# Kernel tuning notes

Hardware: AMD Instinct MI355X
Metric: run time of the kernel (lower is better)

The kernel has to match this reference:

```python
import jax, jax.numpy as jnp
import numpy as np

K1 = 3                      # spline kernel size per pseudo dim
SIZE = float(np.sqrt(2.0))  # pseudo_cartesian normalization size


def spline_weights(p, k):
    """Degree-1 open B-spline basis over 2D pseudo coords.
    p: [..., 2] in [0,1]. Returns basis [..., 4], weight_index [..., 4]."""
    v = jnp.clip(p, 0.0, 1.0) * (k - 1)
    lo = jnp.floor(v)
    frac = v - lo
    lo = lo.astype(jnp.int32)
    off = jnp.array([0, 1], dtype=jnp.int32)
    w0 = jnp.stack([1.0 - frac[..., 0], frac[..., 0]], axis=-1)   # [...,2]
    w1 = jnp.stack([1.0 - frac[..., 1], frac[..., 1]], axis=-1)   # [...,2]
    i0 = jnp.clip(lo[..., 0:1] + off, 0, k - 1)                    # [...,2]
    i1 = jnp.clip(lo[..., 1:2] + off, 0, k - 1)                    # [...,2]
    basis = (w0[..., :, None] * w1[..., None, :]).reshape(*p.shape[:-1], 4)
    widx = (i0[..., :, None] + k * i1[..., None, :]).reshape(*p.shape[:-1], 4)
    return basis, widx


def setup_inputs() -> dict:
    key = jax.random.key(0)
    kx, ke, kp, kq, kw, kb = jax.random.split(key, 6)
    N, C, P, E, K = 50000, 64, 16, 800000, K1 * K1
    x = jax.random.normal(kx, (N, C), dtype=jnp.float32)
    pos = jax.random.uniform(kp, (N, 2), dtype=jnp.float32)
    pose = jax.random.normal(kq, (N, P, 2), dtype=jnp.float32)
    pose = pose / (jnp.linalg.norm(pose, axis=-1, keepdims=True) + 1e-8)  # unit pose vectors
    W = jax.random.normal(kw, (P, K, C), dtype=jnp.float32) / np.sqrt(C * 4.0)
    bias = jax.random.normal(kb, (P,), dtype=jnp.float32) * 0.01
    edge_index = jax.random.randint(ke, (2, E), 0, N, dtype=jnp.int64)
    return {"x": x, "pos": pos, "pose": pose, "W": W, "bias": bias,
            "edge_index": edge_index}


def reference(x, pos, pose, W, bias, edge_index):
    N, C = x.shape
    P = pose.shape[1]
    row, col = edge_index[0], edge_index[1]
    # pseudo_cartesian: normalized relative position in [0,1]^2
    pseudo = (pos[col] - pos[row]) / (2.0 * SIZE) + 0.5              # [E,2]
    # posevec_to_rotmat on detached pose vectors
    pose_c = jax.lax.stop_gradient(pose)
    a, b = pose_c[..., 0], pose_c[..., 1]
    R = jnp.stack([jnp.stack([a, -b], -1), jnp.stack([b, a], -1)], -2)  # [N,P,2,2]
    Re = R[row]                                                      # [E,P,2,2]
    # rotate pseudo coords about (0.5, 0.5), batched over all poses
    p = jnp.einsum('epij,ej->epi', Re, pseudo - 0.5) + 0.5           # [E,P,2]
    basis, widx = spline_weights(p, K1)                              # [E,P,4]
    # SplineConv (out_channels=1, no root weight, no norm):
    # precompute per-node per-pose per-kernel-bin projections
    Z = jnp.einsum('nc,pkc->npk', x, W)                              # [N,P,K]
    pidx = jnp.arange(P)[None, :, None]
    vals = Z[col[:, None, None], pidx, widx]                         # [E,P,4]
    msg = jnp.sum(basis * vals, axis=-1)                             # [E,P]
    out = jax.ops.segment_sum(msg, row, num_segments=N)              # [N,P]
    return out + bias[None, :]
```

## Files before the change

kernel.cpp:

```cpp
#include <hip/hip_runtime.h>
#include <hip/hip_bf16.h>

#define C_DIM 64
#define P_DIM 16
#define K_DIM 9
#define PK (P_DIM * K_DIM)
#define INV2S 0.35355339059327373f

#define ZS_STRIDE 152
#define SH_FLOATS 4864

__global__ __launch_bounds__(256) void z_gemm_kernel(const float* __restrict__ x,
                                                     const float* __restrict__ W,
                                                     const float* __restrict__ bias,
                                                     float* __restrict__ out,
                                                     __hip_bfloat16* __restrict__ Zb,
                                                     int N) {
    __shared__ float sh_raw[SH_FLOATS];
    float (*xs)[C_DIM + 4] = (float(*)[C_DIM + 4])sh_raw;
    __hip_bfloat16* zs = (__hip_bfloat16*)sh_raw;

    const int block_row = blockIdx.x * 64;
    const int tid = threadIdx.x;

    {
        const float4 b4 = ((const float4*)bias)[tid & 3];
        const int o4 = block_row * 4 + tid;
        if (o4 < N * 4) ((float4*)out)[o4] = b4;
    }

    for (int i = tid; i < C_DIM * (C_DIM / 4); i += 256) {
        int r = i >> 4, c4 = i & 15;
        int gr = block_row + r;
        float4 v = make_float4(0.0f, 0.0f, 0.0f, 0.0f);
        if (gr < N) v = ((const float4*)x)[(size_t)gr * (C_DIM / 4) + c4];
        *(float4*)&xs[r][c4 * 4] = v;
    }
    __syncthreads();

    const int rg = tid & 15;
    const int p  = tid >> 4;
    const int j0 = p * K_DIM;

    float acc[4][K_DIM];
    #pragma unroll
    for (int i = 0; i < 4; ++i)
        #pragma unroll
        for (int k = 0; k < K_DIM; ++k) acc[i][k] = 0.0f;

    const float4* W4 = (const float4*)W;
    #pragma unroll 4
    for (int cs = 0; cs < 16; ++cs) {
        float4 xv[4];
        #pragma unroll
        for (int i = 0; i < 4; ++i) xv[i] = *(const float4*)&xs[rg + 16 * i][cs * 4];
        #pragma unroll
        for (int k = 0; k < K_DIM; ++k) {
            float4 wv = W4[(size_t)(j0 + k) * (C_DIM / 4) + cs];
            #pragma unroll
            for (int i = 0; i < 4; ++i) {
                acc[i][k] = fmaf(xv[i].x, wv.x, acc[i][k]);
                acc[i][k] = fmaf(xv[i].y, wv.y, acc[i][k]);
                acc[i][k] = fmaf(xv[i].z, wv.z, acc[i][k]);
                acc[i][k] = fmaf(xv[i].w, wv.w, acc[i][k]);
            }
        }
    }
    __syncthreads();

    #pragma unroll
    for (int i = 0; i < 4; ++i) {
        __hip_bfloat16* zrow = &zs[(rg + 16 * i) * ZS_STRIDE + j0];
        #pragma unroll
        for (int k = 0; k < K_DIM; ++k)
            zrow[k] = __float2bfloat16(acc[i][k]);
    }
    __syncthreads();

    const int nrow = min(64, N - block_row);
    float4* Zb4 = (float4*)Zb;
    for (int i = tid; i < nrow * 18; i += 256) {
        int row = i / 18, q = i - row * 18;
        float4 v = *(const float4*)&zs[row * ZS_STRIDE + q * 8];
        Zb4[(size_t)(block_row + row) * 18 + q] = v;
    }
}

#define EILP 8
__global__ __launch_bounds__(256) void edge_kernel(const int* __restrict__ ei,
                                                   const float* __restrict__ pos,
                                                   const float* __restrict__ pose,
                                                   const __hip_bfloat16* __restrict__ Zb,
                                                   float* __restrict__ out,
                                                   int E) {
    const int p  = threadIdx.x & 15;
    const int eg = threadIdx.x >> 4;
    const int e0 = blockIdx.x * (16 * EILP) + eg;

    int  r[EILP], c[EILP];
    bool valid[EILP];
    #pragma unroll
    for (int it = 0; it < EILP; ++it) {
        int e = e0 + it * 16;
        valid[it] = (e < E);
        int ec = valid[it] ? e : 0;
        r[it] = ei[ec];
        c[it] = ei[E + ec];
    }

    float d0[EILP], d1[EILP];
    #pragma unroll
    for (int it = 0; it < EILP; ++it) {
        const float2 pc = ((const float2*)pos)[c[it]];
        const float2 pr = ((const float2*)pos)[r[it]];
        d0[it] = (pc.x - pr.x) * INV2S;
        d1[it] = (pc.y - pr.y) * INV2S;
    }

    float2 ab[EILP];
    #pragma unroll
    for (int it = 0; it < EILP; ++it)
        ab[it] = ((const float2*)pose)[(size_t)r[it] * P_DIM + p];

    #pragma unroll
    for (int it = 0; it < EILP; ++it) {
        const float p0 = fmaf(ab[it].x, d0[it], fmaf(-ab[it].y, d1[it], 0.5f));
        const float p1 = fmaf(ab[it].y, d0[it], fmaf( ab[it].x, d1[it], 0.5f));

        const float v0 = fminf(fmaxf(p0, 0.0f), 1.0f) * 2.0f;
        const float v1 = fminf(fmaxf(p1, 0.0f), 1.0f) * 2.0f;
        const float lo0 = floorf(v0);
        const float lo1 = floorf(v1);
        const float f0 = v0 - lo0;
        const float f1 = v1 - lo1;
        const int i00 = min((int)lo0, 2);
        const int i01 = min((int)lo0 + 1, 2);
        const int i10 = min((int)lo1, 2);
        const int i11 = min((int)lo1 + 1, 2);

        const __hip_bfloat16* __restrict__ Zp = Zb + (size_t)c[it] * PK + p * K_DIM;
        const float w00 = (1.0f - f0) * (1.0f - f1);
        const float w01 = (1.0f - f0) * f1;
        const float w10 = f0 * (1.0f - f1);
        const float w11 = f0 * f1;

        float m = w00 * __bfloat162float(Zp[i00 + 3 * i10]);
        m = fmaf(w01, __bfloat162float(Zp[i00 + 3 * i11]), m);
        m = fmaf(w10, __bfloat162float(Zp[i01 + 3 * i10]), m);
        m = fmaf(w11, __bfloat162float(Zp[i01 + 3 * i11]), m);

        if (valid[it]) atomicAdd(&out[(size_t)r[it] * P_DIM + p], m);
    }
}

extern "C" void kernel_launch(void* const* d_in, const int* in_sizes, int n_in,
                              void* d_out, int out_size, void* d_ws, size_t ws_size,
                              hipStream_t stream) {
    const float* x    = (const float*)d_in[0];
    const float* pos  = (const float*)d_in[1];
    const float* pose = (const float*)d_in[2];
    const float* W    = (const float*)d_in[3];
    const float* bias = (const float*)d_in[4];
    const int*   ei   = (const int*)d_in[5];

    const int N = in_sizes[0] / C_DIM;
    const int E = in_sizes[5] / 2;

    float* out = (float*)d_out;
    __hip_bfloat16* Zb = (__hip_bfloat16*)d_ws;

    z_gemm_kernel<<<(N + 63) / 64, 256, 0, stream>>>(x, W, bias, out, Zb, N);
    edge_kernel<<<(E + 16 * EILP - 1) / (16 * EILP), 256, 0, stream>>>(ei, pos, pose, Zb, out, E);
}
```

Measured before the change: 156.0 us.

## Use split-bf16 MFMA for Z projection and bf16-packed pose for edge gather

The per-node projection GEMM is rewritten to use MFMA 16x16x32 bf16 instructions, with x and W each split into hi/lo bf16 parts so the product stays near fp32 accuracy. W is converted into shared memory per block, and Z is written straight from the accumulators. The GEMM kernel also packs pose vectors into bf16 pairs in workspace, halving the per-edge pose gather bytes in the edge kernel. This costs extra MFMA passes and redundant W conversion in every block, and pose precision drops to bf16.

Result: faster. 144.7 us (-7.2%).

```diff
diff --git a/kernel.cpp b/kernel.cpp
--- a/kernel.cpp
+++ b/kernel.cpp
@@ -1,5 +1,4 @@
 #include <hip/hip_runtime.h>
-#include <hip/hip_bf16.h>
 
 #define C_DIM 64
 #define P_DIM 16
@@ -7,21 +6,32 @@
 #define PK (P_DIM * K_DIM)
 #define INV2S 0.35355339059327373f
 
-#define ZS_STRIDE 152
-#define SH_FLOATS 4864
+typedef __attribute__((ext_vector_type(8))) short short8v;
+typedef __attribute__((ext_vector_type(4))) float f32x4;
+
+__device__ __forceinline__ ushort f2bf(float f) {
+    uint u = __builtin_bit_cast(uint, f);
+    return (ushort)((u + 0x7FFFu + ((u >> 16) & 1u)) >> 16);
+}
+__device__ __forceinline__ float bf2f(ushort h) {
+    return __builtin_bit_cast(float, ((uint)h) << 16);
+}
+
+#define ZSTRIDE 72
 
 __global__ __launch_bounds__(256) void z_gemm_kernel(const float* __restrict__ x,
                                                      const float* __restrict__ W,
                                                      const float* __restrict__ bias,
+                                                     const float* __restrict__ pose,
                                                      float* __restrict__ out,
-                                                     __hip_bfloat16* __restrict__ Zb,
+                                                     ushort* __restrict__ Zb,
+                                                     uint* __restrict__ pose_bf,
                                                      int N) {
-    __shared__ float sh_raw[SH_FLOATS];
-    float (*xs)[C_DIM + 4] = (float(*)[C_DIM + 4])sh_raw;
-    __hip_bfloat16* zs = (__hip_bfloat16*)sh_raw;
-
+    __shared__ ushort w_hi[PK * ZSTRIDE];
+    __shared__ ushort w_lo[PK * ZSTRIDE];
+
+    const int tid = threadIdx.x;
     const int block_row = blockIdx.x * 64;
-    const int tid = threadIdx.x;
 
     {
         const float4 b4 = ((const float4*)bias)[tid & 3];
@@ -29,68 +39,95 @@
         if (o4 < N * 4) ((float4*)out)[o4] = b4;
     }
 
-    for (int i = tid; i < C_DIM * (C_DIM / 4); i += 256) {
-        int r = i >> 4, c4 = i & 15;
-        int gr = block_row + r;
-        float4 v = make_float4(0.0f, 0.0f, 0.0f, 0.0f);
-        if (gr < N) v = ((const float4*)x)[(size_t)gr * (C_DIM / 4) + c4];
-        *(float4*)&xs[r][c4 * 4] = v;
+    if (pose_bf != nullptr) {
+        for (int i = tid; i < 64 * P_DIM; i += 256) {
+            const int r = block_row + (i >> 4);
+            if (r < N) {
+                const float2 ab = ((const float2*)pose)[(size_t)r * P_DIM + (i & 15)];
+                pose_bf[(size_t)r * P_DIM + (i & 15)] =
+                    (uint)f2bf(ab.x) | ((uint)f2bf(ab.y) << 16);
+            }
+        }
+    }
+
+    for (int i = tid; i < PK * (C_DIM / 2); i += 256) {
+        const int n  = i >> 5;
+        const int k2 = i & 31;
+        const float2 w2 = ((const float2*)W)[i];
+        const int o = n * ZSTRIDE + k2 * 2;
+        const ushort h0 = f2bf(w2.x);
+        const ushort h1 = f2bf(w2.y);
+        w_hi[o]     = h0;
+        w_hi[o + 1] = h1;
+        w_lo[o]     = f2bf(w2.x - bf2f(h0));
+        w_lo[o + 1] = f2bf(w2.y - bf2f(h1));
     }
     __syncthreads();
 
-    const int rg = tid & 15;
-    const int p  = tid >> 4;
-    const int j0 = p * K_DIM;
-
-    float acc[4][K_DIM];
-    #pragma unroll
-    for (int i = 0; i < 4; ++i)
+    const int lane = tid & 63;
+    const int wv   = tid >> 6;
+    const int col  = lane & 15;
+    const int kg   = lane >> 4;
+
+    const int arow = block_row + wv * 16 + col;
+    const float* xr = x + (size_t)(arow < N ? arow : 0) * C_DIM;
+    float4 x0 = ((const float4*)xr)[kg * 2];
+    float4 x1 = ((const float4*)xr)[kg * 2 + 1];
+    float4 x2 = ((const float4*)xr)[8 + kg * 2];
+    float4 x3 = ((const float4*)xr)[8 + kg * 2 + 1];
+    if (arow >= N) {
+        x0 = x1 = x2 = x3 = make_float4(0.f, 0.f, 0.f, 0.f);
+    }
+
+    short8v a_hi0, a_lo0, a_hi1, a_lo1;
+    {
+        const float t0[8] = {x0.x, x0.y, x0.z, x0.w, x1.x, x1.y, x1.z, x1.w};
+        const float t1[8] = {x2.x, x2.y, x2.z, x2.w, x3.x, x3.y, x3.z, x3.w};
         #pragma unroll
-        for (int k = 0; k < K_DIM; ++k) acc[i][k] = 0.0f;
-
-    const float4* W4 = (const float4*)W;
-    #pragma unroll 4
-    for (int cs = 0; cs < 16; ++cs) {
-        float4 xv[4];
+        for (int e = 0; e < 8; ++e) {
+            const ushort h = f2bf(t0[e]);
+            a_hi0[e] = (short)h;
+            a_lo0[e] = (short)f2bf(t0[e] - bf2f(h));
+            const ushort g = f2bf(t1[e]);
+            a_hi1[e] = (short)g;
+            a_lo1[e] = (short)f2bf(t1[e] - bf2f(g));
+        }
+    }
+
+    const int orow0 = block_row + wv * 16 + kg * 4;
+
+    #pragma unroll
+    for (int nt = 0; nt < 9; ++nt) {
+        const ushort* bhp = &w_hi[(nt * 16 + col) * ZSTRIDE + kg * 8];
+        const ushort* blp = &w_lo[(nt * 16 + col) * ZSTRIDE + kg * 8];
+        const short8v bh0 = *(const short8v*)bhp;
+        const short8v bh1 = *(const short8v*)(bhp + 32);
+        const short8v bl0 = *(const short8v*)blp;
+        const short8v bl1 = *(const short8v*)(blp + 32);
+
+        f32x4 acc = {0.f, 0.f, 0.f, 0.f};
+        acc = __builtin_amdgcn_mfma_f32_16x16x32_bf16(a_lo0, bh0, acc, 0, 0, 0);
+        acc = __builtin_amdgcn_mfma_f32_16x16x32_bf16(a_hi0, bl0, acc, 0, 0, 0);
+        acc = __builtin_amdgcn_mfma_f32_16x16x32_bf16(a_lo1, bh1, acc, 0, 0, 0);
+        acc = __builtin_amdgcn_mfma_f32_16x16x32_bf16(a_hi1, bl1, acc, 0, 0, 0);
+        acc = __builtin_amdgcn_mfma_f32_16x16x32_bf16(a_hi0, bh0, acc, 0, 0, 0);
+        acc = __builtin_amdgcn_mfma_f32_16x16x32_bf16(a_hi1, bh1, acc, 0, 0, 0);
+
         #pragma unroll
-        for (int i = 0; i < 4; ++i) xv[i] = *(const float4*)&xs[rg + 16 * i][cs * 4];
-        #pragma unroll
-        for (int k = 0; k < K_DIM; ++k) {
-            float4 wv = W4[(size_t)(j0 + k) * (C_DIM / 4) + cs];
-            #pragma unroll
-            for (int i = 0; i < 4; ++i) {
-                acc[i][k] = fmaf(xv[i].x, wv.x, acc[i][k]);
-                acc[i][k] = fmaf(xv[i].y, wv.y, acc[i][k]);
-                acc[i][k] = fmaf(xv[i].z, wv.z, acc[i][k]);
-                acc[i][k] = fmaf(xv[i].w, wv.w, acc[i][k]);
-            }
-        }
-    }
-    __syncthreads();
-
-    #pragma unroll
-    for (int i = 0; i < 4; ++i) {
-        __hip_bfloat16* zrow = &zs[(rg + 16 * i) * ZS_STRIDE + j0];
-        #pragma unroll
-        for (int k = 0; k < K_DIM; ++k)
-            zrow[k] = __float2bfloat16(acc[i][k]);
-    }
-    __syncthreads();
-
-    const int nrow = min(64, N - block_row);
-    float4* Zb4 = (float4*)Zb;
-    for (int i = tid; i < nrow * 18; i += 256) {
-        int row = i / 18, q = i - row * 18;
-        float4 v = *(const float4*)&zs[row * ZS_STRIDE + q * 8];
-        Zb4[(size_t)(block_row + row) * 18 + q] = v;
+        for (int r = 0; r < 4; ++r) {
+            const int row = orow0 + r;
+            if (row < N) Zb[(size_t)row * PK + nt * 16 + col] = f2bf(acc[r]);
+        }
     }
 }
 
 #define EILP 8
+template <bool USEBF>
 __global__ __launch_bounds__(256) void edge_kernel(const int* __restrict__ ei,
                                                    const float* __restrict__ pos,
                                                    const float* __restrict__ pose,
-                                                   const __hip_bfloat16* __restrict__ Zb,
+                                                   const uint* __restrict__ pose_bf,
+                                                   const ushort* __restrict__ Zb,
                                                    float* __restrict__ out,
                                                    int E) {
     const int p  = threadIdx.x & 15;
@@ -117,15 +154,24 @@
         d1[it] = (pc.y - pr.y) * INV2S;
     }
 
-    float2 ab[EILP];
-    #pragma unroll
-    for (int it = 0; it < EILP; ++it)
-        ab[it] = ((const float2*)pose)[(size_t)r[it] * P_DIM + p];
-
-    #pragma unroll
-    for (int it = 0; it < EILP; ++it) {
-        const float p0 = fmaf(ab[it].x, d0[it], fmaf(-ab[it].y, d1[it], 0.5f));
-        const float p1 = fmaf(ab[it].y, d0[it], fmaf( ab[it].x, d1[it], 0.5f));
+    float a_[EILP], b_[EILP];
+    #pragma unroll
+    for (int it = 0; it < EILP; ++it) {
+        if (USEBF) {
+            const uint ab = pose_bf[(size_t)r[it] * P_DIM + p];
+            a_[it] = bf2f((ushort)(ab & 0xffffu));
+            b_[it] = bf2f((ushort)(ab >> 16));
+        } else {
+            const float2 ab = ((const float2*)pose)[(size_t)r[it] * P_DIM + p];
+            a_[it] = ab.x;
+            b_[it] = ab.y;
+        }
+    }
+
+    #pragma unroll
+    for (int it = 0; it < EILP; ++it) {
+        const float p0 = fmaf(a_[it], d0[it], fmaf(-b_[it], d1[it], 0.5f));
+        const float p1 = fmaf(b_[it], d0[it], fmaf( a_[it], d1[it], 0.5f));
 
         const float v0 = fminf(fmaxf(p0, 0.0f), 1.0f) * 2.0f;
         const float v1 = fminf(fmaxf(p1, 0.0f), 1.0f) * 2.0f;
@@ -138,16 +184,16 @@
         const int i10 = min((int)lo1, 2);
         const int i11 = min((int)lo1 + 1, 2);
 
-        const __hip_bfloat16* __restrict__ Zp = Zb + (size_t)c[it] * PK + p * K_DIM;
+        const ushort* __restrict__ Zp = Zb + (size_t)c[it] * PK + p * K_DIM;
         const float w00 = (1.0f - f0) * (1.0f - f1);
         const float w01 = (1.0f - f0) * f1;
         const float w10 = f0 * (1.0f - f1);
         const float w11 = f0 * f1;
 
-        float m = w00 * __bfloat162float(Zp[i00 + 3 * i10]);
-        m = fmaf(w01, __bfloat162float(Zp[i00 + 3 * i11]), m);
-        m = fmaf(w10, __bfloat162float(Zp[i01 + 3 * i10]), m);
-        m = fmaf(w11, __bfloat162float(Zp[i01 + 3 * i11]), m);
+        float m = w00 * bf2f(Zp[i00 + 3 * i10]);
+        m = fmaf(w01, bf2f(Zp[i00 + 3 * i11]), m);
+        m = fmaf(w10, bf2f(Zp[i01 + 3 * i10]), m);
+        m = fmaf(w11, bf2f(Zp[i01 + 3 * i11]), m);
 
         if (valid[it]) atomicAdd(&out[(size_t)r[it] * P_DIM + p], m);
     }
@@ -167,8 +213,18 @@
     const int E = in_sizes[5] / 2;
 
     float* out = (float*)d_out;
-    __hip_bfloat16* Zb = (__hip_bfloat16*)d_ws;
-
-    z_gemm_kernel<<<(N + 63) / 64, 256, 0, stream>>>(x, W, bias, out, Zb, N);
-    edge_kernel<<<(E + 16 * EILP - 1) / (16 * EILP), 256, 0, stream>>>(ei, pos, pose, Zb, out, E);
-}
+    ushort* Zb = (ushort*)d_ws;
+
+    const size_t zb_bytes   = (size_t)N * PK * sizeof(ushort);
+    const size_t pose_bytes = (size_t)N * P_DIM * sizeof(uint);
+    uint* pose_bf = (ws_size >= zb_bytes + pose_bytes)
+                        ? (uint*)((char*)d_ws + zb_bytes) : nullptr;
+
+    z_gemm_kernel<<<(N + 63) / 64, 256, 0, stream>>>(x, W, bias, pose, out, Zb, pose_bf, N);
+
+    const int eblocks = (E + 16 * EILP - 1) / (16 * EILP);
+    if (pose_bf != nullptr)
+        edge_kernel<true><<<eblocks, 256, 0, stream>>>(ei, pos, pose, pose_bf, Zb, out, E);
+    else
+        edge_kernel<false><<<eblocks, 256, 0, stream>>>(ei, pos, pose, pose_bf, Zb, out, E);
+}
```
